# Optimization experiments

Hardware: AMD Instinct MI355X
Metric: run time of the kernel (lower is better)

Reference implementation:

```python
import jax, jax.numpy as jnp
import numpy as np

N, E, D, G, L, C, NI, NL = 100000, 1600000, 128, 1024, 3, 128, 100000, 64


def setup_inputs() -> dict:
    key = jax.random.key(0)
    ks = jax.random.split(key, 16)
    x = jax.random.normal(ks[0], (N, D), dtype=jnp.float32)
    src = jax.random.randint(ks[1], (E,), 0, N, dtype=jnp.int32)
    dst = jax.random.randint(ks[2], (E,), 0, N, dtype=jnp.int32)
    graph_ids = jnp.sort(jax.random.randint(ks[3], (N,), 0, G, dtype=jnp.int32))
    init_feat = jax.random.normal(ks[4], (NI, D), dtype=jnp.float32)
    init_graph_ids = jnp.sort(jax.random.randint(ks[5], (NI,), 0, G, dtype=jnp.int32))
    lead_feat = jax.random.normal(ks[6], (NL, D), dtype=jnp.float32)
    s = 1.0 / np.sqrt(D)
    W = jax.random.normal(ks[7], (L, D, D), dtype=jnp.float32) * s
    Wc = jax.random.normal(ks[8], (L, D, D), dtype=jnp.float32) * s
    b = jnp.zeros((L, D), dtype=jnp.float32)
    eps = jnp.zeros((L,), dtype=jnp.float32)
    fc1_w = jax.random.normal(ks[9], (D, D), dtype=jnp.float32) * s
    fc1_b = jnp.zeros((D,), dtype=jnp.float32)
    fc2_w = jax.random.normal(ks[10], (D, C), dtype=jnp.float32) * s
    fc2_b = jnp.zeros((C,), dtype=jnp.float32)
    return {"x": x, "src": src, "dst": dst, "graph_ids": graph_ids,
            "init_feat": init_feat, "init_graph_ids": init_graph_ids,
            "lead_feat": lead_feat, "W": W, "Wc": Wc, "b": b, "eps": eps,
            "fc1_w": fc1_w, "fc1_b": fc1_b, "fc2_w": fc2_w, "fc2_b": fc2_b,
            "num_graphs": G}


def reference(x, src, dst, graph_ids, init_feat, init_graph_ids, lead_feat,
              W, Wc, b, eps, fc1_w, fc1_b, fc2_w, fc2_b, num_graphs):
    n_nodes = x.shape[0]
    # global context: per-graph sum pooling of initial graph + lead graph sum
    h_init = jax.ops.segment_sum(init_feat, init_graph_ids, num_segments=num_graphs)  # [G,D]
    h_lead = jnp.sum(lead_feat, axis=0)  # [D]
    ctx = h_init[graph_ids] + h_lead  # [N,D], constant across layers

    h = x
    h_global = jax.ops.segment_sum(h, graph_ids, num_segments=num_graphs)  # [G,D]
    for l in range(W.shape[0]):
        agg = jax.ops.segment_sum(h[src], dst, num_segments=n_nodes)  # neighbor sum [N,D]
        m = (1.0 + eps[l]) * h + agg + h_global[graph_ids]
        h = jax.nn.relu(m @ W[l] + ctx @ Wc[l] + b[l])
        h_global = jax.ops.segment_sum(h, graph_ids, num_segments=num_graphs)
    out = jax.nn.relu(h_global @ fc1_w + fc1_b) @ fc2_w + fc2_b  # [G,C]
    return out
```

## Files before the change

kernel.cpp:

```cpp
#include <hip/hip_runtime.h>

#define D 128

typedef short short8_t __attribute__((ext_vector_type(8)));
typedef float float4_t __attribute__((ext_vector_type(4)));

#define BSH 8
#define BSZ 256
#define NBLK_A 256

__device__ __forceinline__ float bf_lo(unsigned u) { return __uint_as_float(u << 16); }
__device__ __forceinline__ float bf_hi(unsigned u) { return __uint_as_float(u & 0xffff0000u); }
__device__ __forceinline__ unsigned to_bf1(float x) {
    unsigned b = __float_as_uint(x);
    return (b + 0x7fffu + ((b >> 16) & 1u)) >> 16;
}
__device__ __forceinline__ unsigned pack2(float a, float b) {
    return to_bf1(a) | (to_bf1(b) << 16);
}


__global__ void f32_to_bf16(const float4* __restrict__ in, uint2* __restrict__ out, long n4) {
    long i = (long)blockIdx.x * blockDim.x + threadIdx.x;
    long stride = (long)gridDim.x * blockDim.x;
    for (; i < n4; i += stride) {
        float4 v = in[i];
        out[i] = make_uint2(pack2(v.x, v.y), pack2(v.z, v.w));
    }
}

__global__ void wpack(const float* __restrict__ W, uint4* __restrict__ Wpk, int L_) {
    int id = blockIdx.x * blockDim.x + threadIdx.x;
    if (id >= L_ * 2048) return;
    int lane = id & 63, cc = (id >> 6) & 3, t = (id >> 8) & 7, l = id >> 11;
    int n = t * 16 + (lane & 15);
    int k0 = cc * 32 + (lane >> 4) * 8;
    const float* Wb = W + (long)l * D * D;
    unsigned u0 = pack2(Wb[(long)(k0 + 0) * D + n], Wb[(long)(k0 + 1) * D + n]);
    unsigned u1 = pack2(Wb[(long)(k0 + 2) * D + n], Wb[(long)(k0 + 3) * D + n]);
    unsigned u2 = pack2(Wb[(long)(k0 + 4) * D + n], Wb[(long)(k0 + 5) * D + n]);
    unsigned u3 = pack2(Wb[(long)(k0 + 6) * D + n], Wb[(long)(k0 + 7) * D + n]);
    Wpk[id] = make_uint4(u0, u1, u2, u3);
}


__global__ __launch_bounds__(256)
void csr_hist(const int* __restrict__ dst, int* __restrict__ Hist, int E_, int chunk) {
    __shared__ int h[512];
    int b = blockIdx.x, t = threadIdx.x;
    h[t] = 0; h[t + 256] = 0;
    __syncthreads();
    int base = b * chunk;
    int end = base + chunk; if (end > E_) end = E_;
    for (int i = base + t; i < end; i += 256)
        atomicAdd(&h[dst[i] >> BSH], 1);
    __syncthreads();
    Hist[b * 512 + t] = h[t];
    Hist[b * 512 + t + 256] = h[t + 256];
}

__global__ __launch_bounds__(256)
void csr_scan_blocks(int* __restrict__ Hist, int* __restrict__ Tot) {
    __shared__ int sc[256];
    int bkt = blockIdx.x, t = threadIdx.x;
    int v = Hist[t * 512 + bkt];
    sc[t] = v; __syncthreads();
    for (int off = 1; off < 256; off <<= 1) {
        int u = (t >= off) ? sc[t - off] : 0;
        __syncthreads();
        sc[t] += u;
        __syncthreads();
    }
    Hist[t * 512 + bkt] = sc[t] - v;
    if (t == 255) Tot[bkt] = sc[255];
}

__global__ __launch_bounds__(512)
void csr_scan_base(const int* __restrict__ Tot, int* __restrict__ Base, int NB) {
    __shared__ int sc[512];
    int t = threadIdx.x;
    int v = (t < NB) ? Tot[t] : 0;
    sc[t] = v; __syncthreads();
    for (int off = 1; off < 512; off <<= 1) {
        int u = (t >= off) ? sc[t - off] : 0;
        __syncthreads();
        sc[t] += u;
        __syncthreads();
    }
    Base[t] = sc[t] - v;
    if (t == NB - 1) Base[NB] = sc[t];
}

__global__ __launch_bounds__(256)
void csr_scatter(const int* __restrict__ src, const int* __restrict__ dst,
                 const int* __restrict__ Hist, const int* __restrict__ Base,
                 unsigned* __restrict__ EdgeBuf, int E_, int chunk) {
    __shared__ int cur[512];
    int b = blockIdx.x, t = threadIdx.x;
    cur[t]       = Base[t]       + Hist[b * 512 + t];
    cur[t + 256] = Base[t + 256] + Hist[b * 512 + t + 256];
    __syncthreads();
    int base = b * chunk;
    int end = base + chunk; if (end > E_) end = E_;
    for (int i = base + t; i < end; i += 256) {
        int s = src[i], dd = dst[i];
        int p = atomicAdd(&cur[dd >> BSH], 1);
        EdgeBuf[p] = (unsigned)s | ((unsigned)(dd & (BSZ - 1)) << 24);
    }
}

__global__ __launch_bounds__(256)
void csr_fill(const unsigned* __restrict__ EdgeBuf, const int* __restrict__ Base,
              int* __restrict__ rowptr, int* __restrict__ csr, int N_, int E_) {
    __shared__ int deg[256];
    __shared__ int cur[256];
    int b = blockIdx.x, t = threadIdx.x;
    int e0 = Base[b], e1 = Base[b + 1];
    deg[t] = 0;
    __syncthreads();
    for (int i = e0 + t; i < e1; i += 256)
        atomicAdd(&deg[EdgeBuf[i] >> 24], 1);
    __syncthreads();
    int v = deg[t];
    cur[t] = v; __syncthreads();
    for (int off = 1; off < 256; off <<= 1) {
        int u = (t >= off) ? cur[t - off] : 0;
        __syncthreads();
        cur[t] += u;
        __syncthreads();
    }
    int excl = cur[t] - v;
    int node = b * BSZ + t;
    if (node < N_) rowptr[node] = e0 + excl;
    cur[t] = e0 + excl;
    __syncthreads();
    for (int i = e0 + t; i < e1; i += 256) {
        unsigned ev = EdgeBuf[i];
        int p = atomicAdd(&cur[ev >> 24], 1);
        csr[p] = (int)(ev & 0x00FFFFFFu);
    }
    if (b == 0 && t == 0) rowptr[N_] = E_;
}

__global__ void find_starts(const int* __restrict__ gids, int n, int G_,
                            int* __restrict__ start) {
    int g = blockIdx.x * blockDim.x + threadIdx.x;
    if (g > G_) return;
    if (g == G_) { start[g] = n; return; }
    int lo = 0, hi = n;
    while (lo < hi) { int mid = (lo + hi) >> 1; if (gids[mid] < g) lo = mid + 1; else hi = mid; }
    start[g] = lo;
}


__global__ void reduce_lead(const float* __restrict__ lead, float* __restrict__ hlead, int NL) {
    int d = threadIdx.x;
    float a0 = 0.f, a1 = 0.f, a2 = 0.f, a3 = 0.f;
    int r = 0;
    for (; r + 4 <= NL; r += 4) {
        a0 += lead[(long)r * D + d];
        a1 += lead[(long)(r + 1) * D + d];
        a2 += lead[(long)(r + 2) * D + d];
        a3 += lead[(long)(r + 3) * D + d];
    }
    for (; r < NL; ++r) a0 += lead[(long)r * D + d];
    hlead[d] = a0 + a1 + a2 + a3;
}

__global__ __launch_bounds__(128)
void segsum_pg(const float* __restrict__ feat, const int* __restrict__ start,
               const float* __restrict__ addv, float* __restrict__ out) {
    int g = blockIdx.x;
    int d = threadIdx.x;
    int r0 = start[g], r1 = start[g + 1];
    float a0 = 0.f, a1 = 0.f, a2 = 0.f, a3 = 0.f;
    int r = r0;
    for (; r + 4 <= r1; r += 4) {
        a0 += feat[(long)r * D + d];
        a1 += feat[(long)(r + 1) * D + d];
        a2 += feat[(long)(r + 2) * D + d];
        a3 += feat[(long)(r + 3) * D + d];
    }
    for (; r < r1; ++r) a0 += feat[(long)r * D + d];
    float s = a0 + a1 + a2 + a3;
    if (addv) s += addv[d];
    out[(long)g * D + d] = s;
}

__global__ __launch_bounds__(128)
void graph_term(const unsigned* __restrict__ hb, const int* __restrict__ start,
                const float* __restrict__ ctx, const float* __restrict__ Wl,
                const float* __restrict__ Wcl, const float* __restrict__ bl,
                float* __restrict__ T) {
    __shared__ float xs[D];
    __shared__ float cs[D];
    int g = blockIdx.x, tid = threadIdx.x;
    int r0 = start[g], r1 = start[g + 1];
    int c = tid >> 1;
    bool hi = tid & 1;
    float a0=0,a1=0,a2=0,a3=0,a4=0,a5=0,a6=0,a7=0;
    int r = r0;
    for (; r + 8 <= r1; r += 8) {
        unsigned u0 = hb[(long)(r+0)*64+c], u1 = hb[(long)(r+1)*64+c];
        unsigned u2 = hb[(long)(r+2)*64+c], u3 = hb[(long)(r+3)*64+c];
        unsigned u4 = hb[(long)(r+4)*64+c], u5 = hb[(long)(r+5)*64+c];
        unsigned u6 = hb[(long)(r+6)*64+c], u7 = hb[(long)(r+7)*64+c];
        a0 += hi ? bf_hi(u0) : bf_lo(u0);
        a1 += hi ? bf_hi(u1) : bf_lo(u1);
        a2 += hi ? bf_hi(u2) : bf_lo(u2);
        a3 += hi ? bf_hi(u3) : bf_lo(u3);
        a4 += hi ? bf_hi(u4) : bf_lo(u4);
        a5 += hi ? bf_hi(u5) : bf_lo(u5);
        a6 += hi ? bf_hi(u6) : bf_lo(u6);
        a7 += hi ? bf_hi(u7) : bf_lo(u7);
    }
    for (; r < r1; ++r) {
        unsigned u = hb[(long)r*64+c];
        a0 += hi ? bf_hi(u) : bf_lo(u);
    }
    xs[tid] = ((a0+a1)+(a2+a3)) + ((a4+a5)+(a6+a7));
    cs[tid] = ctx[(long)g * D + tid];
    __syncthreads();
    float p0=0,p1=0,p2=0,p3=0;
    for (int k = 0; k < D; k += 4) {
        p0 += xs[k]   * Wl[(long)k*D + tid];
        p1 += xs[k+1] * Wl[(long)(k+1)*D + tid];
        p2 += xs[k+2] * Wl[(long)(k+2)*D + tid];
        p3 += xs[k+3] * Wl[(long)(k+3)*D + tid];
    }
    for (int k = 0; k < D; k += 4) {
        p0 += cs[k]   * Wcl[(long)k*D + tid];
        p1 += cs[k+1] * Wcl[(long)(k+1)*D + tid];
        p2 += cs[k+2] * Wcl[(long)(k+2)*D + tid];
        p3 += cs[k+3] * Wcl[(long)(k+3)*D + tid];
    }
    T[(long)g * D + tid] = bl[tid] + (p0 + p1) + (p2 + p3);
}

__global__ __launch_bounds__(128)
void readout(const unsigned* __restrict__ hb, const int* __restrict__ start,
             const float* __restrict__ f1w, const float* __restrict__ f1b,
             const float* __restrict__ f2w, const float* __restrict__ f2b,
             float* __restrict__ out) {
    __shared__ float xs[D];
    __shared__ float zs[D];
    int g = blockIdx.x, tid = threadIdx.x;
    int r0 = start[g], r1 = start[g + 1];
    int c = tid >> 1;
    bool hi = tid & 1;
    float a0=0,a1=0,a2=0,a3=0;
    int r = r0;
    for (; r + 4 <= r1; r += 4) {
        unsigned u0 = hb[(long)(r+0)*64+c], u1 = hb[(long)(r+1)*64+c];
        unsigned u2 = hb[(long)(r+2)*64+c], u3 = hb[(long)(r+3)*64+c];
        a0 += hi ? bf_hi(u0) : bf_lo(u0);
        a1 += hi ? bf_hi(u1) : bf_lo(u1);
        a2 += hi ? bf_hi(u2) : bf_lo(u2);
        a3 += hi ? bf_hi(u3) : bf_lo(u3);
    }
    for (; r < r1; ++r) {
        unsigned u = hb[(long)r*64+c];
        a0 += hi ? bf_hi(u) : bf_lo(u);
    }
    xs[tid] = (a0+a1)+(a2+a3);
    __syncthreads();
    float p0=0,p1=0,p2=0,p3=0;
    for (int k = 0; k < D; k += 4) {
        p0 += xs[k]   * f1w[(long)k*D + tid];
        p1 += xs[k+1] * f1w[(long)(k+1)*D + tid];
        p2 += xs[k+2] * f1w[(long)(k+2)*D + tid];
        p3 += xs[k+3] * f1w[(long)(k+3)*D + tid];
    }
    zs[tid] = fmaxf(f1b[tid] + (p0+p1)+(p2+p3), 0.f);
    __syncthreads();
    float q0=0,q1=0,q2=0,q3=0;
    for (int k = 0; k < D; k += 4) {
        q0 += zs[k]   * f2w[(long)k*D + tid];
        q1 += zs[k+1] * f2w[(long)(k+1)*D + tid];
        q2 += zs[k+2] * f2w[(long)(k+2)*D + tid];
        q3 += zs[k+3] * f2w[(long)(k+3)*D + tid];
    }
    out[(long)g * D + tid] = f2b[tid] + (q0+q1)+(q2+q3);
}

#define TROWS 64
__global__ __launch_bounds__(256, 6)
void layer_kernel(const unsigned* __restrict__ hb, const uint4* __restrict__ Wpk_l,
                  const float* __restrict__ T, const int* __restrict__ gids,
                  const int* __restrict__ rowptr, const int* __restrict__ csr,
                  const float* __restrict__ eps_l, unsigned* __restrict__ houtb, int n) {
    __shared__ __align__(16) unsigned Minb[TROWS][68];
    int tid = threadIdx.x;
    int w = tid >> 6, lane = tid & 63;
    int w16 = w * 16;
    int rowBase = blockIdx.x * TROWS;
    int rb = rowBase + w16;
    float epsv = 1.0f + *eps_l;

    int rp = rb + lane; if (rp > n) rp = n;
    int evv = rowptr[rp];

    int e0 = __shfl(evv, 0);
    int e1 = __shfl(evv, 1);
    int idxv = (e0 + lane < e1) ? csr[e0 + lane] : 0;

    for (int i = 0; i < 16; ++i) {
        int r = rb + i;
        int deg = e1 - e0;
        int e0n = __shfl(evv, i + 1);
        int e1n = __shfl(evv, i + 2);
        int idxn = (e0n + lane < e1n) ? csr[e0n + lane] : 0;
        float sx = 0.f, sy = 0.f;
        if (r < n) {
            unsigned su = hb[(long)r * 64 + lane];
            float ax0 = epsv * bf_lo(su), ay0 = epsv * bf_hi(su);
            float ax1=0,ay1=0,ax2=0,ay2=0,ax3=0,ay3=0;
            int iv = idxv;
            int base = 0;
            while (true) {
                int m = deg - base; if (m > 64) m = 64;
                int j = 0;
                for (; j + 8 <= m; j += 8) {
                    int s0=__shfl(iv,j+0), s1=__shfl(iv,j+1), s2=__shfl(iv,j+2), s3=__shfl(iv,j+3);
                    int s4=__shfl(iv,j+4), s5=__shfl(iv,j+5), s6=__shfl(iv,j+6), s7=__shfl(iv,j+7);
                    unsigned u0=hb[(long)s0*64+lane], u1=hb[(long)s1*64+lane];
                    unsigned u2=hb[(long)s2*64+lane], u3=hb[(long)s3*64+lane];
                    unsigned u4=hb[(long)s4*64+lane], u5=hb[(long)s5*64+lane];
                    unsigned u6=hb[(long)s6*64+lane], u7=hb[(long)s7*64+lane];
                    ax0+=bf_lo(u0); ay0+=bf_hi(u0); ax1+=bf_lo(u1); ay1+=bf_hi(u1);
                    ax2+=bf_lo(u2); ay2+=bf_hi(u2); ax3+=bf_lo(u3); ay3+=bf_hi(u3);
                    ax0+=bf_lo(u4); ay0+=bf_hi(u4); ax1+=bf_lo(u5); ay1+=bf_hi(u5);
                    ax2+=bf_lo(u6); ay2+=bf_hi(u6); ax3+=bf_lo(u7); ay3+=bf_hi(u7);
                }
                for (; j < m; ++j) {
                    int s = __shfl(iv, j);
                    unsigned u = hb[(long)s * 64 + lane];
                    ax0 += bf_lo(u); ay0 += bf_hi(u);
                }
                base += 64;
                if (base >= deg) break;
                int mm = deg - base;
                iv = (lane < mm) ? csr[e0 + base + lane] : 0;
            }
            sx = (ax0 + ax1) + (ax2 + ax3);
            sy = (ay0 + ay1) + (ay2 + ay3);
        }
        Minb[w16 + i][lane] = pack2(sx, sy);
        e0 = e0n; e1 = e1n; idxv = idxn;
    }

    int m_ = lane & 15, quad = lane >> 4;
    float4_t acc[8];
    #pragma unroll
    for (int tt = 0; tt < 8; ++tt) { acc[tt][0]=0.f; acc[tt][1]=0.f; acc[tt][2]=0.f; acc[tt][3]=0.f; }

    #pragma unroll
    for (int cc = 0; cc < 4; ++cc) {
        short8_t af = *(const short8_t*)&Minb[w16 + m_][cc * 16 + quad * 4];
        #pragma unroll
        for (int tt = 0; tt < 8; ++tt) {
            short8_t bf = *(const short8_t*)&Wpk_l[(tt * 4 + cc) * 64 + lane];
            acc[tt] = __builtin_amdgcn_mfma_f32_16x16x32_bf16(af, bf, acc[tt], 0, 0, 0);
        }
    }

    int gq[4];
    #pragma unroll
    for (int reg = 0; reg < 4; ++reg) {
        int r = rb + quad * 4 + reg;
        gq[reg] = (r < n) ? gids[r] : 0;
    }
    #pragma unroll
    for (int tt = 0; tt < 8; ++tt) {
        int col = tt * 16 + m_;
        #pragma unroll
        for (int reg = 0; reg < 4; ++reg) {
            float v = acc[tt][reg] + T[(long)gq[reg] * D + col];
            v = fmaxf(v, 0.f);
            float v2 = __shfl_xor(v, 1);
            if (!(lane & 1)) Minb[w16 + quad * 4 + reg][tt * 8 + (m_ >> 1)] = pack2(v, v2);
        }
    }
    #pragma unroll
    for (int rr = 0; rr < 4; ++rr) {
        int lrow = rr * 4 + (lane >> 4);
        int r = rowBase + w16 + lrow;
        if (r < n) {
            uint4 v = *(const uint4*)&Minb[w16 + lrow][(lane & 15) * 4];
            *(uint4*)&houtb[(long)r * 64 + (lane & 15) * 4] = v;
        }
    }
}


static inline size_t align512(size_t x) { return (x + 511) & ~(size_t)511; }

extern "C" void kernel_launch(void* const* d_in, const int* in_sizes, int n_in,
                              void* d_out, int out_size, void* d_ws, size_t ws_size,
                              hipStream_t stream) {
    const float* x        = (const float*)d_in[0];
    const int*   src      = (const int*)d_in[1];
    const int*   dst      = (const int*)d_in[2];
    const int*   gids     = (const int*)d_in[3];
    const float* initf    = (const float*)d_in[4];
    const int*   init_gid = (const int*)d_in[5];
    const float* leadf    = (const float*)d_in[6];
    const float* W        = (const float*)d_in[7];
    const float* Wc       = (const float*)d_in[8];
    const float* b        = (const float*)d_in[9];
    const float* eps      = (const float*)d_in[10];
    const float* fc1_w    = (const float*)d_in[11];
    const float* fc1_b    = (const float*)d_in[12];
    const float* fc2_w    = (const float*)d_in[13];
    const float* fc2_b    = (const float*)d_in[14];
    float* out = (float*)d_out;

    const int N  = in_sizes[0] / D;
    const int E  = in_sizes[1];
    const int NL = in_sizes[6] / D;
    const int L  = in_sizes[10];

    char* p = (char*)d_ws;
    unsigned* xb  = (unsigned*)p; p += align512((size_t)N * 64 * 4);
    unsigned* hAb = (unsigned*)p; p += align512((size_t)N * 64 * 4);
    unsigned* hBb = (unsigned*)p; p += align512((size_t)N * 64 * 4);
    const int G = 1024;
    float* T     = (float*)p; p += align512((size_t)G * D * 4);
    float* ctx   = (float*)p; p += align512((size_t)G * D * 4);
    float* hlead = (float*)p; p += align512((size_t)D * 4);
    int* rowptr  = (int*)p;   p += align512((size_t)(N + 1) * 4);
    int* csr     = (int*)p;   p += align512((size_t)E * 4);
    unsigned* EdgeBuf = (unsigned*)p; p += align512((size_t)E * 4);
    int* Hist    = (int*)p;   p += align512((size_t)NBLK_A * 512 * 4);
    int* Tot     = (int*)p;   p += align512((size_t)520 * 4);
    int* Base    = (int*)p;   p += align512((size_t)520 * 4);
    int* nstart  = (int*)p;   p += align512((size_t)(G + 1) * 4);
    int* istart  = (int*)p;   p += align512((size_t)(G + 1) * 4);
    uint4* Wpk   = (uint4*)p; p += align512((size_t)L * 2048 * 16);
    (void)ws_size; (void)n_in;

    const int NB = (N + BSZ - 1) / BSZ;
    const int chunk = (E + NBLK_A - 1) / NBLK_A;

    csr_hist<<<NBLK_A, 256, 0, stream>>>(dst, Hist, E, chunk);
    csr_scan_blocks<<<NB, 256, 0, stream>>>(Hist, Tot);
    csr_scan_base<<<1, 512, 0, stream>>>(Tot, Base, NB);
    csr_scatter<<<NBLK_A, 256, 0, stream>>>(src, dst, Hist, Base, EdgeBuf, E, chunk);
    csr_fill<<<NB, 256, 0, stream>>>(EdgeBuf, Base, rowptr, csr, N, E);

    f32_to_bf16<<<2048, 256, 0, stream>>>((const float4*)x, (uint2*)xb, (long)N * D / 4);
    wpack<<<(L * 2048 + 255) / 256, 256, 0, stream>>>(W, Wpk, L);

    find_starts<<<(G + 256) / 256, 256, 0, stream>>>(gids, N, G, nstart);
    find_starts<<<(G + 256) / 256, 256, 0, stream>>>(init_gid, in_sizes[4] / D, G, istart);

    reduce_lead<<<1, D, 0, stream>>>(leadf, hlead, NL);
    segsum_pg<<<G, D, 0, stream>>>(initf, istart, hlead, ctx);

    const unsigned* hcur = xb;
    unsigned* bufs[2] = { hAb, hBb };
    int layerBlocks = (N + TROWS - 1) / TROWS;
    for (int l = 0; l < L; ++l) {
        graph_term<<<G, D, 0, stream>>>(hcur, nstart, ctx, W + (long)l * D * D,
                                        Wc + (long)l * D * D, b + (long)l * D, T);
        unsigned* hnext = bufs[l & 1];
        layer_kernel<<<layerBlocks, 256, 0, stream>>>(hcur, Wpk + (size_t)l * 2048, T,
                                                      gids, rowptr, csr,
                                                      eps + l, hnext, N);
        hcur = hnext;
    }

    readout<<<G, D, 0, stream>>>(hcur, nstart, fc1_w, fc1_b, fc2_w, fc2_b, out);
}
```

Baseline: 534.9 us.

## Split graph term into segsum plus batched GEMMs and precompute context projection

Replaces the per-graph graph_term kernel with a segment-sum kernel that writes bf16 per-graph sums, a GEMM batched over 8 graphs per block for the W term, and a single upfront ctx_gemm that precomputes ctx@Wc+b for all layers. This reuses weight loads across several graphs instead of re-reading the full weight matrix per graph, and removes the repeated context projection from every layer. The segment sums are also reworked so each thread reads both halves of a packed word with two row-halves in parallel. Two find_starts launches are merged into one. The cost is an extra launch per layer, extra workspace, and bf16 rounding of the graph sums before the GEMM.

```diff
diff --git a/kernel.cpp b/kernel.cpp
--- a/kernel.cpp
+++ b/kernel.cpp
@@ -142,14 +142,18 @@
     if (b == 0 && t == 0) rowptr[N_] = E_;
 }
 
-__global__ void find_starts(const int* __restrict__ gids, int n, int G_,
-                            int* __restrict__ start) {
-    int g = blockIdx.x * blockDim.x + threadIdx.x;
-    if (g > G_) return;
-    if (g == G_) { start[g] = n; return; }
+__global__ void find_starts2(const int* __restrict__ g1, int n1,
+                             const int* __restrict__ g2, int n2,
+                             int G_, int* __restrict__ s1, int* __restrict__ s2) {
+    int id = blockIdx.x * blockDim.x + threadIdx.x;
+    if (id >= 2 * (G_ + 1)) return;
+    const int* arr; int n; int* out; int g;
+    if (id <= G_) { arr = g1; n = n1; out = s1; g = id; }
+    else { arr = g2; n = n2; out = s2; g = id - (G_ + 1); }
+    if (g == G_) { out[g] = n; return; }
     int lo = 0, hi = n;
-    while (lo < hi) { int mid = (lo + hi) >> 1; if (gids[mid] < g) lo = mid + 1; else hi = mid; }
-    start[g] = lo;
+    while (lo < hi) { int mid = (lo + hi) >> 1; if (arr[mid] < g) lo = mid + 1; else hi = mid; }
+    out[g] = lo;
 }
 
 
@@ -188,53 +192,97 @@
 }
 
 __global__ __launch_bounds__(128)
-void graph_term(const unsigned* __restrict__ hb, const int* __restrict__ start,
-                const float* __restrict__ ctx, const float* __restrict__ Wl,
-                const float* __restrict__ Wcl, const float* __restrict__ bl,
-                float* __restrict__ T) {
-    __shared__ float xs[D];
-    __shared__ float cs[D];
-    int g = blockIdx.x, tid = threadIdx.x;
+void segsum_h(const unsigned* __restrict__ hb, const int* __restrict__ start,
+              unsigned* __restrict__ hgb) {
+    __shared__ float part[2][64][2];
+    int g = blockIdx.x, t = threadIdx.x;
+    int c = t & 63, half = t >> 6;
     int r0 = start[g], r1 = start[g + 1];
-    int c = tid >> 1;
-    bool hi = tid & 1;
-    float a0=0,a1=0,a2=0,a3=0,a4=0,a5=0,a6=0,a7=0;
-    int r = r0;
-    for (; r + 8 <= r1; r += 8) {
-        unsigned u0 = hb[(long)(r+0)*64+c], u1 = hb[(long)(r+1)*64+c];
-        unsigned u2 = hb[(long)(r+2)*64+c], u3 = hb[(long)(r+3)*64+c];
-        unsigned u4 = hb[(long)(r+4)*64+c], u5 = hb[(long)(r+5)*64+c];
-        unsigned u6 = hb[(long)(r+6)*64+c], u7 = hb[(long)(r+7)*64+c];
-        a0 += hi ? bf_hi(u0) : bf_lo(u0);
-        a1 += hi ? bf_hi(u1) : bf_lo(u1);
-        a2 += hi ? bf_hi(u2) : bf_lo(u2);
-        a3 += hi ? bf_hi(u3) : bf_lo(u3);
-        a4 += hi ? bf_hi(u4) : bf_lo(u4);
-        a5 += hi ? bf_hi(u5) : bf_lo(u5);
-        a6 += hi ? bf_hi(u6) : bf_lo(u6);
-        a7 += hi ? bf_hi(u7) : bf_lo(u7);
-    }
-    for (; r < r1; ++r) {
-        unsigned u = hb[(long)r*64+c];
-        a0 += hi ? bf_hi(u) : bf_lo(u);
-    }
-    xs[tid] = ((a0+a1)+(a2+a3)) + ((a4+a5)+(a6+a7));
-    cs[tid] = ctx[(long)g * D + tid];
-    __syncthreads();
-    float p0=0,p1=0,p2=0,p3=0;
-    for (int k = 0; k < D; k += 4) {
-        p0 += xs[k]   * Wl[(long)k*D + tid];
-        p1 += xs[k+1] * Wl[(long)(k+1)*D + tid];
-        p2 += xs[k+2] * Wl[(long)(k+2)*D + tid];
-        p3 += xs[k+3] * Wl[(long)(k+3)*D + tid];
-    }
-    for (int k = 0; k < D; k += 4) {
-        p0 += cs[k]   * Wcl[(long)k*D + tid];
-        p1 += cs[k+1] * Wcl[(long)(k+1)*D + tid];
-        p2 += cs[k+2] * Wcl[(long)(k+2)*D + tid];
-        p3 += cs[k+3] * Wcl[(long)(k+3)*D + tid];
-    }
-    T[(long)g * D + tid] = bl[tid] + (p0 + p1) + (p2 + p3);
+    float l0=0,h0=0,l1=0,h1=0,l2=0,h2=0,l3=0,h3=0;
+    int r = r0 + half;
+    for (; r + 6 < r1; r += 8) {
+        unsigned a = hb[(long)r * 64 + c];
+        unsigned bq = hb[(long)(r + 2) * 64 + c];
+        unsigned cq = hb[(long)(r + 4) * 64 + c];
+        unsigned dq = hb[(long)(r + 6) * 64 + c];
+        l0 += bf_lo(a);  h0 += bf_hi(a);
+        l1 += bf_lo(bq); h1 += bf_hi(bq);
+        l2 += bf_lo(cq); h2 += bf_hi(cq);
+        l3 += bf_lo(dq); h3 += bf_hi(dq);
+    }
+    for (; r < r1; r += 2) { unsigned a = hb[(long)r * 64 + c]; l0 += bf_lo(a); h0 += bf_hi(a); }
+    part[half][c][0] = (l0 + l1) + (l2 + l3);
+    part[half][c][1] = (h0 + h1) + (h2 + h3);
+    __syncthreads();
+    if (t < 64) {
+        float lo = part[0][t][0] + part[1][t][0];
+        float hi = part[0][t][1] + part[1][t][1];
+        hgb[(long)g * 64 + t] = pack2(lo, hi);
+    }
+}
+
+__global__ __launch_bounds__(256)
+void ctx_gemm(const float* __restrict__ cvec, const float* __restrict__ Wc,
+              const float* __restrict__ bb, float* __restrict__ ctxT, int Gtot) {
+    __shared__ float xs[8][D];
+    int bi = blockIdx.x;
+    int bpl = Gtot >> 3;
+    int l = bi / bpl;
+    int gb = (bi - l * bpl) * 8;
+    int tid = threadIdx.x;
+    for (int u = tid; u < 8 * D; u += 256)
+        xs[u >> 7][u & 127] = cvec[(long)(gb + (u >> 7)) * D + (u & 127)];
+    __syncthreads();
+    int col = tid & 127, half = tid >> 7;
+    const float* Wl = Wc + (long)l * D * D;
+    const float* x0 = xs[half * 4 + 0];
+    const float* x1 = xs[half * 4 + 1];
+    const float* x2 = xs[half * 4 + 2];
+    const float* x3 = xs[half * 4 + 3];
+    float p0 = 0.f, p1 = 0.f, p2 = 0.f, p3 = 0.f;
+    #pragma unroll 4
+    for (int k = 0; k < D; ++k) {
+        float wv = Wl[(long)k * D + col];
+        p0 += x0[k] * wv; p1 += x1[k] * wv;
+        p2 += x2[k] * wv; p3 += x3[k] * wv;
+    }
+    float bv = bb[l * D + col];
+    long ob = ((long)l * Gtot + gb + half * 4) * D + col;
+    ctxT[ob]         = p0 + bv;
+    ctxT[ob + D]     = p1 + bv;
+    ctxT[ob + 2 * D] = p2 + bv;
+    ctxT[ob + 3 * D] = p3 + bv;
+}
+
+__global__ __launch_bounds__(256)
+void hg_gemm(const unsigned* __restrict__ hgb, const float* __restrict__ Wl,
+             const float* __restrict__ ctxT_l, float* __restrict__ T) {
+    __shared__ float xs[8][D];
+    int gb = blockIdx.x * 8;
+    int tid = threadIdx.x;
+    for (int u = tid; u < 8 * 64; u += 256) {
+        unsigned v = hgb[(long)gb * 64 + u];
+        xs[u >> 6][(u & 63) * 2]     = bf_lo(v);
+        xs[u >> 6][(u & 63) * 2 + 1] = bf_hi(v);
+    }
+    __syncthreads();
+    int col = tid & 127, half = tid >> 7;
+    const float* x0 = xs[half * 4 + 0];
+    const float* x1 = xs[half * 4 + 1];
+    const float* x2 = xs[half * 4 + 2];
+    const float* x3 = xs[half * 4 + 3];
+    float p0 = 0.f, p1 = 0.f, p2 = 0.f, p3 = 0.f;
+    #pragma unroll 4
+    for (int k = 0; k < D; ++k) {
+        float wv = Wl[(long)k * D + col];
+        p0 += x0[k] * wv; p1 += x1[k] * wv;
+        p2 += x2[k] * wv; p3 += x3[k] * wv;
+    }
+    long ob = (long)(gb + half * 4) * D + col;
+    T[ob]         = p0 + ctxT_l[ob];
+    T[ob + D]     = p1 + ctxT_l[ob + D];
+    T[ob + 2 * D] = p2 + ctxT_l[ob + 2 * D];
+    T[ob + 3 * D] = p3 + ctxT_l[ob + 3 * D];
 }
 
 __global__ __launch_bounds__(128)
@@ -242,45 +290,43 @@
              const float* __restrict__ f1w, const float* __restrict__ f1b,
              const float* __restrict__ f2w, const float* __restrict__ f2b,
              float* __restrict__ out) {
+    __shared__ float part[2][64][2];
     __shared__ float xs[D];
     __shared__ float zs[D];
-    int g = blockIdx.x, tid = threadIdx.x;
+    int g = blockIdx.x, t = threadIdx.x;
+    int c = t & 63, half = t >> 6;
     int r0 = start[g], r1 = start[g + 1];
-    int c = tid >> 1;
-    bool hi = tid & 1;
-    float a0=0,a1=0,a2=0,a3=0;
-    int r = r0;
-    for (; r + 4 <= r1; r += 4) {
-        unsigned u0 = hb[(long)(r+0)*64+c], u1 = hb[(long)(r+1)*64+c];
-        unsigned u2 = hb[(long)(r+2)*64+c], u3 = hb[(long)(r+3)*64+c];
-        a0 += hi ? bf_hi(u0) : bf_lo(u0);
-        a1 += hi ? bf_hi(u1) : bf_lo(u1);
-        a2 += hi ? bf_hi(u2) : bf_lo(u2);
-        a3 += hi ? bf_hi(u3) : bf_lo(u3);
-    }
-    for (; r < r1; ++r) {
-        unsigned u = hb[(long)r*64+c];
-        a0 += hi ? bf_hi(u) : bf_lo(u);
-    }
-    xs[tid] = (a0+a1)+(a2+a3);
+    float l0=0,h0=0,l1=0,h1=0;
+    int r = r0 + half;
+    for (; r + 2 < r1; r += 4) {
+        unsigned a = hb[(long)r * 64 + c];
+        unsigned bq = hb[(long)(r + 2) * 64 + c];
+        l0 += bf_lo(a);  h0 += bf_hi(a);
+        l1 += bf_lo(bq); h1 += bf_hi(bq);
+    }
+    if (r < r1) { unsigned a = hb[(long)r * 64 + c]; l0 += bf_lo(a); h0 += bf_hi(a); }
+    part[half][c][0] = l0 + l1;
+    part[half][c][1] = h0 + h1;
+    __syncthreads();
+    xs[t] = part[0][t >> 1][t & 1] + part[1][t >> 1][t & 1];
     __syncthreads();
     float p0=0,p1=0,p2=0,p3=0;
     for (int k = 0; k < D; k += 4) {
-        p0 += xs[k]   * f1w[(long)k*D + tid];
-        p1 += xs[k+1] * f1w[(long)(k+1)*D + tid];
-        p2 += xs[k+2] * f1w[(long)(k+2)*D + tid];
-        p3 += xs[k+3] * f1w[(long)(k+3)*D + tid];
-    }
-    zs[tid] = fmaxf(f1b[tid] + (p0+p1)+(p2+p3), 0.f);
+        p0 += xs[k]     * f1w[(long)k * D + t];
+        p1 += xs[k + 1] * f1w[(long)(k + 1) * D + t];
+        p2 += xs[k + 2] * f1w[(long)(k + 2) * D + t];
+        p3 += xs[k + 3] * f1w[(long)(k + 3) * D + t];
+    }
+    zs[t] = fmaxf(f1b[t] + (p0 + p1) + (p2 + p3), 0.f);
     __syncthreads();
     float q0=0,q1=0,q2=0,q3=0;
     for (int k = 0; k < D; k += 4) {
-        q0 += zs[k]   * f2w[(long)k*D + tid];
-        q1 += zs[k+1] * f2w[(long)(k+1)*D + tid];
-        q2 += zs[k+2] * f2w[(long)(k+2)*D + tid];
-        q3 += zs[k+3] * f2w[(long)(k+3)*D + tid];
-    }
-    out[(long)g * D + tid] = f2b[tid] + (q0+q1)+(q2+q3);
+        q0 += zs[k]     * f2w[(long)k * D + t];
+        q1 += zs[k + 1] * f2w[(long)(k + 1) * D + t];
+        q2 += zs[k + 2] * f2w[(long)(k + 2) * D + t];
+        q3 += zs[k + 3] * f2w[(long)(k + 3) * D + t];
+    }
+    out[(long)g * D + t] = f2b[t] + (q0 + q1) + (q2 + q3);
 }
 
 #define TROWS 64
@@ -417,6 +463,7 @@
 
     const int N  = in_sizes[0] / D;
     const int E  = in_sizes[1];
+    const int NI = in_sizes[4] / D;
     const int NL = in_sizes[6] / D;
     const int L  = in_sizes[10];
 
@@ -426,8 +473,10 @@
     unsigned* hBb = (unsigned*)p; p += align512((size_t)N * 64 * 4);
     const int G = 1024;
     float* T     = (float*)p; p += align512((size_t)G * D * 4);
-    float* ctx   = (float*)p; p += align512((size_t)G * D * 4);
+    float* ctxT  = (float*)p; p += align512((size_t)L * G * D * 4);
+    float* cvec  = (float*)p; p += align512((size_t)G * D * 4);
     float* hlead = (float*)p; p += align512((size_t)D * 4);
+    unsigned* hgb = (unsigned*)p; p += align512((size_t)G * 64 * 4);
     int* rowptr  = (int*)p;   p += align512((size_t)(N + 1) * 4);
     int* csr     = (int*)p;   p += align512((size_t)E * 4);
     unsigned* EdgeBuf = (unsigned*)p; p += align512((size_t)E * 4);
@@ -450,19 +499,20 @@
 
     f32_to_bf16<<<2048, 256, 0, stream>>>((const float4*)x, (uint2*)xb, (long)N * D / 4);
     wpack<<<(L * 2048 + 255) / 256, 256, 0, stream>>>(W, Wpk, L);
-
-    find_starts<<<(G + 256) / 256, 256, 0, stream>>>(gids, N, G, nstart);
-    find_starts<<<(G + 256) / 256, 256, 0, stream>>>(init_gid, in_sizes[4] / D, G, istart);
+    find_starts2<<<(2 * (G + 1) + 255) / 256, 256, 0, stream>>>(gids, N, init_gid, NI,
+                                                                G, nstart, istart);
 
     reduce_lead<<<1, D, 0, stream>>>(leadf, hlead, NL);
-    segsum_pg<<<G, D, 0, stream>>>(initf, istart, hlead, ctx);
+    segsum_pg<<<G, D, 0, stream>>>(initf, istart, hlead, cvec);
+    ctx_gemm<<<L * (G / 8), 256, 0, stream>>>(cvec, Wc, b, ctxT, G);
 
     const unsigned* hcur = xb;
     unsigned* bufs[2] = { hAb, hBb };
     int layerBlocks = (N + TROWS - 1) / TROWS;
     for (int l = 0; l < L; ++l) {
-        graph_term<<<G, D, 0, stream>>>(hcur, nstart, ctx, W + (long)l * D * D,
-                                        Wc + (long)l * D * D, b + (long)l * D, T);
+        segsum_h<<<G, 128, 0, stream>>>(hcur, nstart, hgb);
+        hg_gemm<<<G / 8, 256, 0, stream>>>(hgb, W + (long)l * D * D,
+                                           ctxT + (long)l * G * D, T);
         unsigned* hnext = bufs[l & 1];
         layer_kernel<<<layerBlocks, 256, 0, stream>>>(hcur, Wpk + (size_t)l * 2048, T,
                                                       gids, rowptr, csr,
@@ -470,5 +520,5 @@
         hcur = hnext;
     }
 
-    readout<<<G, D, 0, stream>>>(hcur, nstart, fc1_w, fc1_b, fc2_w, fc2_b, out);
-}
+    readout<<<G, 128, 0, stream>>>(hcur, nstart, fc1_w, fc1_b, fc2_w, fc2_b, out);
+}
```

Result: slower. 558.9 us (+4.5%).

## Merge preprocessing kernels into fewer launches and widen neighbor gather unroll

Applied to the files above, without the earlier changes.

Folds the histogram, bf16 conversion, weight packing, segment-start searches and lead reduction into one multi-role kernel. The init-feature segment sum is folded into the edge scatter kernel, which cuts the launch count from about eleven setup kernels to five. The readout reduction now splits rows across two half-blocks, and the neighbor gather adds a 16-way unrolled load batch to raise memory-level parallelism. The risks are higher register pressure in the layer kernel and shared-memory allocation from the idle roles in the fused kernels.

```diff
diff --git a/kernel.cpp b/kernel.cpp
--- a/kernel.cpp
+++ b/kernel.cpp
@@ -19,45 +19,75 @@
     return to_bf1(a) | (to_bf1(b) << 16);
 }
 
-
-__global__ void f32_to_bf16(const float4* __restrict__ in, uint2* __restrict__ out, long n4) {
-    long i = (long)blockIdx.x * blockDim.x + threadIdx.x;
-    long stride = (long)gridDim.x * blockDim.x;
-    for (; i < n4; i += stride) {
-        float4 v = in[i];
-        out[i] = make_uint2(pack2(v.x, v.y), pack2(v.z, v.w));
-    }
-}
-
-__global__ void wpack(const float* __restrict__ W, uint4* __restrict__ Wpk, int L_) {
-    int id = blockIdx.x * blockDim.x + threadIdx.x;
-    if (id >= L_ * 2048) return;
-    int lane = id & 63, cc = (id >> 6) & 3, t = (id >> 8) & 7, l = id >> 11;
-    int n = t * 16 + (lane & 15);
-    int k0 = cc * 32 + (lane >> 4) * 8;
-    const float* Wb = W + (long)l * D * D;
-    unsigned u0 = pack2(Wb[(long)(k0 + 0) * D + n], Wb[(long)(k0 + 1) * D + n]);
-    unsigned u1 = pack2(Wb[(long)(k0 + 2) * D + n], Wb[(long)(k0 + 3) * D + n]);
-    unsigned u2 = pack2(Wb[(long)(k0 + 4) * D + n], Wb[(long)(k0 + 5) * D + n]);
-    unsigned u3 = pack2(Wb[(long)(k0 + 6) * D + n], Wb[(long)(k0 + 7) * D + n]);
-    Wpk[id] = make_uint4(u0, u1, u2, u3);
-}
-
-
 __global__ __launch_bounds__(256)
-void csr_hist(const int* __restrict__ dst, int* __restrict__ Hist, int E_, int chunk) {
-    __shared__ int h[512];
+void prep1(const int* __restrict__ dst, int* __restrict__ Hist, int E_, int chunk,
+           const float4* __restrict__ x4, uint2* __restrict__ xb2, long n4,
+           const float* __restrict__ W, uint4* __restrict__ Wpk, int L_,
+           const int* __restrict__ gids, int N_, const int* __restrict__ init_gid, int NI_,
+           int G_, int* __restrict__ nstart, int* __restrict__ istart,
+           const float* __restrict__ leadf, int NL_, float* __restrict__ hlead,
+           int eb1, int eb2, int eb3) {
     int b = blockIdx.x, t = threadIdx.x;
-    h[t] = 0; h[t + 256] = 0;
-    __syncthreads();
-    int base = b * chunk;
-    int end = base + chunk; if (end > E_) end = E_;
-    for (int i = base + t; i < end; i += 256)
-        atomicAdd(&h[dst[i] >> BSH], 1);
-    __syncthreads();
-    Hist[b * 512 + t] = h[t];
-    Hist[b * 512 + t + 256] = h[t + 256];
-}
+    if (b < NBLK_A) {
+        __shared__ int h[512];
+        h[t] = 0; h[t + 256] = 0;
+        __syncthreads();
+        int base = b * chunk;
+        int end = base + chunk; if (end > E_) end = E_;
+        for (int i = base + t; i < end; i += 256)
+            atomicAdd(&h[dst[i] >> BSH], 1);
+        __syncthreads();
+        Hist[b * 512 + t] = h[t];
+        Hist[b * 512 + t + 256] = h[t + 256];
+    } else if (b < eb1) {
+        long i = (long)(b - NBLK_A) * 256 + t;
+        long stride = (long)(eb1 - NBLK_A) * 256;
+        for (; i < n4; i += stride) {
+            float4 v = x4[i];
+            xb2[i] = make_uint2(pack2(v.x, v.y), pack2(v.z, v.w));
+        }
+    } else if (b < eb2) {
+        int id = (b - eb1) * 256 + t;
+        if (id < L_ * 2048) {
+            int lane = id & 63, cc = (id >> 6) & 3, tt = (id >> 8) & 7, l = id >> 11;
+            int n = tt * 16 + (lane & 15);
+            int k0 = cc * 32 + (lane >> 4) * 8;
+            const float* Wb = W + (long)l * D * D;
+            unsigned u0 = pack2(Wb[(long)(k0 + 0) * D + n], Wb[(long)(k0 + 1) * D + n]);
+            unsigned u1 = pack2(Wb[(long)(k0 + 2) * D + n], Wb[(long)(k0 + 3) * D + n]);
+            unsigned u2 = pack2(Wb[(long)(k0 + 4) * D + n], Wb[(long)(k0 + 5) * D + n]);
+            unsigned u3 = pack2(Wb[(long)(k0 + 6) * D + n], Wb[(long)(k0 + 7) * D + n]);
+            Wpk[id] = make_uint4(u0, u1, u2, u3);
+        }
+    } else if (b < eb3) {
+        int id = (b - eb2) * 256 + t;
+        if (id < 2 * (G_ + 1)) {
+            const int* arr; int n; int* outp; int g;
+            if (id <= G_) { arr = gids; n = N_; outp = nstart; g = id; }
+            else { arr = init_gid; n = NI_; outp = istart; g = id - (G_ + 1); }
+            if (g == G_) outp[g] = n;
+            else {
+                int lo = 0, hi = n;
+                while (lo < hi) { int mid = (lo + hi) >> 1; if (arr[mid] < g) lo = mid + 1; else hi = mid; }
+                outp[g] = lo;
+            }
+        }
+    } else {
+        if (t < D) {
+            float a0 = 0.f, a1 = 0.f, a2 = 0.f, a3 = 0.f;
+            int r = 0;
+            for (; r + 4 <= NL_; r += 4) {
+                a0 += leadf[(long)r * D + t];
+                a1 += leadf[(long)(r + 1) * D + t];
+                a2 += leadf[(long)(r + 2) * D + t];
+                a3 += leadf[(long)(r + 3) * D + t];
+            }
+            for (; r < NL_; ++r) a0 += leadf[(long)r * D + t];
+            hlead[t] = a0 + a1 + a2 + a3;
+        }
+    }
+}
+
 
 __global__ __launch_bounds__(256)
 void csr_scan_blocks(int* __restrict__ Hist, int* __restrict__ Tot) {
@@ -92,21 +122,43 @@
 }
 
 __global__ __launch_bounds__(256)
-void csr_scatter(const int* __restrict__ src, const int* __restrict__ dst,
-                 const int* __restrict__ Hist, const int* __restrict__ Base,
-                 unsigned* __restrict__ EdgeBuf, int E_, int chunk) {
-    __shared__ int cur[512];
+void phase3(const int* __restrict__ src, const int* __restrict__ dst,
+            const int* __restrict__ Hist, const int* __restrict__ Base,
+            unsigned* __restrict__ EdgeBuf, int E_, int chunk,
+            const float* __restrict__ initf, const int* __restrict__ istart,
+            const float* __restrict__ hlead, float* __restrict__ cvec, int G_) {
     int b = blockIdx.x, t = threadIdx.x;
-    cur[t]       = Base[t]       + Hist[b * 512 + t];
-    cur[t + 256] = Base[t + 256] + Hist[b * 512 + t + 256];
-    __syncthreads();
-    int base = b * chunk;
-    int end = base + chunk; if (end > E_) end = E_;
-    for (int i = base + t; i < end; i += 256) {
-        int s = src[i], dd = dst[i];
-        int p = atomicAdd(&cur[dd >> BSH], 1);
-        EdgeBuf[p] = (unsigned)s | ((unsigned)(dd & (BSZ - 1)) << 24);
-    }
+    if (b < NBLK_A) {
+        __shared__ int cur[512];
+        cur[t]       = Base[t]       + Hist[b * 512 + t];
+        cur[t + 256] = Base[t + 256] + Hist[b * 512 + t + 256];
+        __syncthreads();
+        int base = b * chunk;
+        int end = base + chunk; if (end > E_) end = E_;
+        for (int i = base + t; i < end; i += 256) {
+            int s = src[i], dd = dst[i];
+            int p = atomicAdd(&cur[dd >> BSH], 1);
+            EdgeBuf[p] = (unsigned)s | ((unsigned)(dd & (BSZ - 1)) << 24);
+        }
+        return;
+    }
+    int g = b - NBLK_A;
+    if (g >= G_) return;
+    __shared__ float xs2[2][D];
+    int col = t & 127, rp = t >> 7;
+    int r0 = istart[g], r1 = istart[g + 1];
+    float a0 = 0.f, a1 = 0.f, a2 = 0.f, a3 = 0.f;
+    int r = r0 + rp;
+    for (; r + 6 < r1; r += 8) {
+        a0 += initf[(long)r * D + col];
+        a1 += initf[(long)(r + 2) * D + col];
+        a2 += initf[(long)(r + 4) * D + col];
+        a3 += initf[(long)(r + 6) * D + col];
+    }
+    for (; r < r1; r += 2) a0 += initf[(long)r * D + col];
+    xs2[rp][col] = (a0 + a1) + (a2 + a3);
+    __syncthreads();
+    if (t < D) cvec[(long)g * D + t] = xs2[0][t] + xs2[1][t] + hlead[t];
 }
 
 __global__ __launch_bounds__(256)
@@ -142,54 +194,9 @@
     if (b == 0 && t == 0) rowptr[N_] = E_;
 }
 
-__global__ void find_starts(const int* __restrict__ gids, int n, int G_,
-                            int* __restrict__ start) {
-    int g = blockIdx.x * blockDim.x + threadIdx.x;
-    if (g > G_) return;
-    if (g == G_) { start[g] = n; return; }
-    int lo = 0, hi = n;
-    while (lo < hi) { int mid = (lo + hi) >> 1; if (gids[mid] < g) lo = mid + 1; else hi = mid; }
-    start[g] = lo;
-}
-
-
-__global__ void reduce_lead(const float* __restrict__ lead, float* __restrict__ hlead, int NL) {
-    int d = threadIdx.x;
-    float a0 = 0.f, a1 = 0.f, a2 = 0.f, a3 = 0.f;
-    int r = 0;
-    for (; r + 4 <= NL; r += 4) {
-        a0 += lead[(long)r * D + d];
-        a1 += lead[(long)(r + 1) * D + d];
-        a2 += lead[(long)(r + 2) * D + d];
-        a3 += lead[(long)(r + 3) * D + d];
-    }
-    for (; r < NL; ++r) a0 += lead[(long)r * D + d];
-    hlead[d] = a0 + a1 + a2 + a3;
-}
-
 __global__ __launch_bounds__(128)
-void segsum_pg(const float* __restrict__ feat, const int* __restrict__ start,
-               const float* __restrict__ addv, float* __restrict__ out) {
-    int g = blockIdx.x;
-    int d = threadIdx.x;
-    int r0 = start[g], r1 = start[g + 1];
-    float a0 = 0.f, a1 = 0.f, a2 = 0.f, a3 = 0.f;
-    int r = r0;
-    for (; r + 4 <= r1; r += 4) {
-        a0 += feat[(long)r * D + d];
-        a1 += feat[(long)(r + 1) * D + d];
-        a2 += feat[(long)(r + 2) * D + d];
-        a3 += feat[(long)(r + 3) * D + d];
-    }
-    for (; r < r1; ++r) a0 += feat[(long)r * D + d];
-    float s = a0 + a1 + a2 + a3;
-    if (addv) s += addv[d];
-    out[(long)g * D + d] = s;
-}
-
-__global__ __launch_bounds__(128)
-void graph_term(const unsigned* __restrict__ hb, const int* __restrict__ start,
-                const float* __restrict__ ctx, const float* __restrict__ Wl,
+void graph_side(const unsigned* __restrict__ hb, const int* __restrict__ start,
+                const float* __restrict__ cvec, const float* __restrict__ Wl,
                 const float* __restrict__ Wcl, const float* __restrict__ bl,
                 float* __restrict__ T) {
     __shared__ float xs[D];
@@ -219,7 +226,7 @@
         a0 += hi ? bf_hi(u) : bf_lo(u);
     }
     xs[tid] = ((a0+a1)+(a2+a3)) + ((a4+a5)+(a6+a7));
-    cs[tid] = ctx[(long)g * D + tid];
+    cs[tid] = cvec[(long)g * D + tid];
     __syncthreads();
     float p0=0,p1=0,p2=0,p3=0;
     for (int k = 0; k < D; k += 4) {
@@ -242,45 +249,43 @@
              const float* __restrict__ f1w, const float* __restrict__ f1b,
              const float* __restrict__ f2w, const float* __restrict__ f2b,
              float* __restrict__ out) {
+    __shared__ float part[2][64][2];
     __shared__ float xs[D];
     __shared__ float zs[D];
-    int g = blockIdx.x, tid = threadIdx.x;
+    int g = blockIdx.x, t = threadIdx.x;
+    int c = t & 63, half = t >> 6;
     int r0 = start[g], r1 = start[g + 1];
-    int c = tid >> 1;
-    bool hi = tid & 1;
-    float a0=0,a1=0,a2=0,a3=0;
-    int r = r0;
-    for (; r + 4 <= r1; r += 4) {
-        unsigned u0 = hb[(long)(r+0)*64+c], u1 = hb[(long)(r+1)*64+c];
-        unsigned u2 = hb[(long)(r+2)*64+c], u3 = hb[(long)(r+3)*64+c];
-        a0 += hi ? bf_hi(u0) : bf_lo(u0);
-        a1 += hi ? bf_hi(u1) : bf_lo(u1);
-        a2 += hi ? bf_hi(u2) : bf_lo(u2);
-        a3 += hi ? bf_hi(u3) : bf_lo(u3);
-    }
-    for (; r < r1; ++r) {
-        unsigned u = hb[(long)r*64+c];
-        a0 += hi ? bf_hi(u) : bf_lo(u);
-    }
-    xs[tid] = (a0+a1)+(a2+a3);
+    float l0=0,h0=0,l1=0,h1=0;
+    int r = r0 + half;
+    for (; r + 2 < r1; r += 4) {
+        unsigned a = hb[(long)r * 64 + c];
+        unsigned bq = hb[(long)(r + 2) * 64 + c];
+        l0 += bf_lo(a);  h0 += bf_hi(a);
+        l1 += bf_lo(bq); h1 += bf_hi(bq);
+    }
+    if (r < r1) { unsigned a = hb[(long)r * 64 + c]; l0 += bf_lo(a); h0 += bf_hi(a); }
+    part[half][c][0] = l0 + l1;
+    part[half][c][1] = h0 + h1;
+    __syncthreads();
+    xs[t] = part[0][t >> 1][t & 1] + part[1][t >> 1][t & 1];
     __syncthreads();
     float p0=0,p1=0,p2=0,p3=0;
     for (int k = 0; k < D; k += 4) {
-        p0 += xs[k]   * f1w[(long)k*D + tid];
-        p1 += xs[k+1] * f1w[(long)(k+1)*D + tid];
-        p2 += xs[k+2] * f1w[(long)(k+2)*D + tid];
-        p3 += xs[k+3] * f1w[(long)(k+3)*D + tid];
-    }
-    zs[tid] = fmaxf(f1b[tid] + (p0+p1)+(p2+p3), 0.f);
+        p0 += xs[k]     * f1w[(long)k * D + t];
+        p1 += xs[k + 1] * f1w[(long)(k + 1) * D + t];
+        p2 += xs[k + 2] * f1w[(long)(k + 2) * D + t];
+        p3 += xs[k + 3] * f1w[(long)(k + 3) * D + t];
+    }
+    zs[t] = fmaxf(f1b[t] + (p0 + p1) + (p2 + p3), 0.f);
     __syncthreads();
     float q0=0,q1=0,q2=0,q3=0;
     for (int k = 0; k < D; k += 4) {
-        q0 += zs[k]   * f2w[(long)k*D + tid];
-        q1 += zs[k+1] * f2w[(long)(k+1)*D + tid];
-        q2 += zs[k+2] * f2w[(long)(k+2)*D + tid];
-        q3 += zs[k+3] * f2w[(long)(k+3)*D + tid];
-    }
-    out[(long)g * D + tid] = f2b[tid] + (q0+q1)+(q2+q3);
+        q0 += zs[k]     * f2w[(long)k * D + t];
+        q1 += zs[k + 1] * f2w[(long)(k + 1) * D + t];
+        q2 += zs[k + 2] * f2w[(long)(k + 2) * D + t];
+        q3 += zs[k + 3] * f2w[(long)(k + 3) * D + t];
+    }
+    out[(long)g * D + t] = f2b[t] + (q0 + q1) + (q2 + q3);
 }
 
 #define TROWS 64
@@ -320,6 +325,28 @@
             while (true) {
                 int m = deg - base; if (m > 64) m = 64;
                 int j = 0;
+                for (; j + 16 <= m; j += 16) {
+                    int s0=__shfl(iv,j+0),  s1=__shfl(iv,j+1),  s2=__shfl(iv,j+2),  s3=__shfl(iv,j+3);
+                    int s4=__shfl(iv,j+4),  s5=__shfl(iv,j+5),  s6=__shfl(iv,j+6),  s7=__shfl(iv,j+7);
+                    int s8=__shfl(iv,j+8),  s9=__shfl(iv,j+9),  sA=__shfl(iv,j+10), sB=__shfl(iv,j+11);
+                    int sC=__shfl(iv,j+12), sD=__shfl(iv,j+13), sE=__shfl(iv,j+14), sF=__shfl(iv,j+15);
+                    unsigned u0=hb[(long)s0*64+lane], u1=hb[(long)s1*64+lane];
+                    unsigned u2=hb[(long)s2*64+lane], u3=hb[(long)s3*64+lane];
+                    unsigned u4=hb[(long)s4*64+lane], u5=hb[(long)s5*64+lane];
+                    unsigned u6=hb[(long)s6*64+lane], u7=hb[(long)s7*64+lane];
+                    unsigned u8=hb[(long)s8*64+lane], u9=hb[(long)s9*64+lane];
+                    unsigned uA=hb[(long)sA*64+lane], uB=hb[(long)sB*64+lane];
+                    unsigned uC=hb[(long)sC*64+lane], uD=hb[(long)sD*64+lane];
+                    unsigned uE=hb[(long)sE*64+lane], uF=hb[(long)sF*64+lane];
+                    ax0+=bf_lo(u0); ay0+=bf_hi(u0); ax1+=bf_lo(u1); ay1+=bf_hi(u1);
+                    ax2+=bf_lo(u2); ay2+=bf_hi(u2); ax3+=bf_lo(u3); ay3+=bf_hi(u3);
+                    ax0+=bf_lo(u4); ay0+=bf_hi(u4); ax1+=bf_lo(u5); ay1+=bf_hi(u5);
+                    ax2+=bf_lo(u6); ay2+=bf_hi(u6); ax3+=bf_lo(u7); ay3+=bf_hi(u7);
+                    ax0+=bf_lo(u8); ay0+=bf_hi(u8); ax1+=bf_lo(u9); ay1+=bf_hi(u9);
+                    ax2+=bf_lo(uA); ay2+=bf_hi(uA); ax3+=bf_lo(uB); ay3+=bf_hi(uB);
+                    ax0+=bf_lo(uC); ay0+=bf_hi(uC); ax1+=bf_lo(uD); ay1+=bf_hi(uD);
+                    ax2+=bf_lo(uE); ay2+=bf_hi(uE); ax3+=bf_lo(uF); ay3+=bf_hi(uF);
+                }
                 for (; j + 8 <= m; j += 8) {
                     int s0=__shfl(iv,j+0), s1=__shfl(iv,j+1), s2=__shfl(iv,j+2), s3=__shfl(iv,j+3);
                     int s4=__shfl(iv,j+4), s5=__shfl(iv,j+5), s6=__shfl(iv,j+6), s7=__shfl(iv,j+7);
@@ -417,16 +444,18 @@
 
     const int N  = in_sizes[0] / D;
     const int E  = in_sizes[1];
+    const int NI = in_sizes[4] / D;
     const int NL = in_sizes[6] / D;
     const int L  = in_sizes[10];
+    const int C  = in_sizes[13] / D;
+    const int G  = out_size / C;
 
     char* p = (char*)d_ws;
     unsigned* xb  = (unsigned*)p; p += align512((size_t)N * 64 * 4);
     unsigned* hAb = (unsigned*)p; p += align512((size_t)N * 64 * 4);
     unsigned* hBb = (unsigned*)p; p += align512((size_t)N * 64 * 4);
-    const int G = 1024;
     float* T     = (float*)p; p += align512((size_t)G * D * 4);
-    float* ctx   = (float*)p; p += align512((size_t)G * D * 4);
+    float* cvec  = (float*)p; p += align512((size_t)G * D * 4);
     float* hlead = (float*)p; p += align512((size_t)D * 4);
     int* rowptr  = (int*)p;   p += align512((size_t)(N + 1) * 4);
     int* csr     = (int*)p;   p += align512((size_t)E * 4);
@@ -442,26 +471,30 @@
     const int NB = (N + BSZ - 1) / BSZ;
     const int chunk = (E + NBLK_A - 1) / NBLK_A;
 
-    csr_hist<<<NBLK_A, 256, 0, stream>>>(dst, Hist, E, chunk);
+    const int CVB = 2048;
+    const int WPB = (L * 2048 + 255) / 256;
+    const int STB = (2 * (G + 1) + 255) / 256;
+    const int eb1 = NBLK_A + CVB;
+    const int eb2 = eb1 + WPB;
+    const int eb3 = eb2 + STB;
+    const int prepBlocks = eb3 + 1;
+
+    prep1<<<prepBlocks, 256, 0, stream>>>(dst, Hist, E, chunk,
+                                          (const float4*)x, (uint2*)xb, (long)N * D / 4,
+                                          W, Wpk, L,
+                                          gids, N, init_gid, NI, G, nstart, istart,
+                                          leadf, NL, hlead, eb1, eb2, eb3);
     csr_scan_blocks<<<NB, 256, 0, stream>>>(Hist, Tot);
     csr_scan_base<<<1, 512, 0, stream>>>(Tot, Base, NB);
-    csr_scatter<<<NBLK_A, 256, 0, stream>>>(src, dst, Hist, Base, EdgeBuf, E, chunk);
+    phase3<<<NBLK_A + G, 256, 0, stream>>>(src, dst, Hist, Base, EdgeBuf, E, chunk,
+                                           initf, istart, hlead, cvec, G);
     csr_fill<<<NB, 256, 0, stream>>>(EdgeBuf, Base, rowptr, csr, N, E);
-
-    f32_to_bf16<<<2048, 256, 0, stream>>>((const float4*)x, (uint2*)xb, (long)N * D / 4);
-    wpack<<<(L * 2048 + 255) / 256, 256, 0, stream>>>(W, Wpk, L);
-
-    find_starts<<<(G + 256) / 256, 256, 0, stream>>>(gids, N, G, nstart);
-    find_starts<<<(G + 256) / 256, 256, 0, stream>>>(init_gid, in_sizes[4] / D, G, istart);
-
-    reduce_lead<<<1, D, 0, stream>>>(leadf, hlead, NL);
-    segsum_pg<<<G, D, 0, stream>>>(initf, istart, hlead, ctx);
 
     const unsigned* hcur = xb;
     unsigned* bufs[2] = { hAb, hBb };
     int layerBlocks = (N + TROWS - 1) / TROWS;
     for (int l = 0; l < L; ++l) {
-        graph_term<<<G, D, 0, stream>>>(hcur, nstart, ctx, W + (long)l * D * D,
+        graph_side<<<G, D, 0, stream>>>(hcur, nstart, cvec, W + (long)l * D * D,
                                         Wc + (long)l * D * D, b + (long)l * D, T);
         unsigned* hnext = bufs[l & 1];
         layer_kernel<<<layerBlocks, 256, 0, stream>>>(hcur, Wpk + (size_t)l * 2048, T,
```

After: 591.8 us. 1.11x slower.
